# Optimization experiments

Measured on AMD Instinct MI355X. Metric: run time of the kernel, lower is better.

## Reference

```python
import jax, jax.numpy as jnp
import numpy as np

D_MODEL = 512
HEADS = 8
D_K = D_MODEL // HEADS
D_FF = 2048
SEQ = 2048
BATCH = 8


def setup_inputs() -> dict:
    key = jax.random.key(0)
    ks = jax.random.split(key, 16)
    xavier = lambda k, shape: jax.random.uniform(
        k, shape, jnp.float32,
        -jnp.sqrt(6.0 / (shape[-2] + shape[-1])), jnp.sqrt(6.0 / (shape[-2] + shape[-1])))
    inp = {
        'x': jax.random.normal(ks[0], (SEQ, BATCH, D_MODEL), jnp.float32),
        'Wq': xavier(ks[1], (D_MODEL, D_MODEL)), 'bq': jnp.zeros((D_MODEL,)),
        'Wv': xavier(ks[2], (D_MODEL, D_MODEL)), 'bv': jnp.zeros((D_MODEL,)),
        'Wr': xavier(ks[3], (D_MODEL, D_MODEL)), 'br': jnp.zeros((D_MODEL,)),
        'W_h': xavier(ks[4], (HEADS, D_K, D_K)),
        'Wo': xavier(ks[5], (D_MODEL, D_MODEL)),
        'bo': jax.random.normal(ks[6], (D_MODEL,)) * 0.01,
        'ln1_g': jnp.ones((D_MODEL,)), 'ln1_b': jnp.zeros((D_MODEL,)),
        'Wf1': xavier(ks[7], (D_MODEL, D_FF)), 'bf1': jnp.zeros((D_FF,)),
        'Wf2': xavier(ks[8], (D_FF, D_MODEL)), 'bf2': jnp.zeros((D_MODEL,)),
        'ln2_g': jnp.ones((D_MODEL,)), 'ln2_b': jnp.zeros((D_MODEL,)),
    }
    return inp


def _layernorm(x, g, b, eps=1e-5):
    mu = jnp.mean(x, axis=-1, keepdims=True)
    var = jnp.var(x, axis=-1, keepdims=True)
    return (x - mu) * jax.lax.rsqrt(var + eps) * g + b


def _forward(x, Wq, bq, Wv, bv, Wr, br, W_h, Wo, bo, ln1_g, ln1_b, Wf1, bf1, Wf2, bf2, ln2_g, ln2_b):
    S, B, D = x.shape
    # causal mask: triu bool ADDED to scores (torch quirk: bool->float gives +1.0)
    mask = jnp.triu(jnp.ones((S, S), jnp.float32), k=1)
    xt = jnp.transpose(x, (1, 0, 2))  # (B, S, D)
    Q = (xt @ Wq.T + bq).reshape(B, S, HEADS, D_K).transpose(0, 2, 1, 3)  # bhsd
    V = (xt @ Wv.T + bv).reshape(B, S, HEADS, D_K).transpose(0, 2, 1, 3)
    Rp = (xt @ Wr.T + br).reshape(B, S, HEADS, D_K).transpose(0, 2, 1, 3)
    # recurrence: h_t = tanh(einsum('hnk,bhn->bhn', W_h, h) + R_t)
    # note: einsum sums W_h over k per (h,n) -> elementwise scale by W_h.sum(-1)
    w_diag = jnp.sum(W_h, axis=-1)  # (H, D_K)

    def step(h, r_t):
        h_new = jnp.tanh(h * w_diag + r_t)
        return h_new, h_new

    h0 = jnp.zeros((B, HEADS, D_K), x.dtype)
    _, H = jax.lax.scan(step, h0, jnp.transpose(Rp, (2, 0, 1, 3)))  # (S,B,H,Dk)
    H = jnp.transpose(H, (1, 2, 0, 3))  # (B,H,S,Dk)
    scale = 1.0 / np.sqrt(D_K)
    scores = jnp.einsum('bhqd,bhkd->bhqk', Q, H) * scale + mask
    attn = jax.nn.softmax(scores, axis=-1)
    out = jnp.einsum('bhqk,bhkd->bhqd', attn, V)
    out = out.transpose(0, 2, 1, 3).reshape(B, S, D)
    attn_out = out @ Wo.T + bo
    attn_out = jnp.transpose(attn_out, (1, 0, 2))  # back to (S,B,D)
    x1 = _layernorm(x + attn_out, ln1_g, ln1_b)
    ff = jax.nn.relu(x1 @ Wf1) + 0.0
    ff = (jax.nn.relu(x1 @ Wf1 + bf1)) @ Wf2 + bf2
    return _layernorm(x1 + ff, ln2_g, ln2_b)


def reference(x, Wq, bq, Wv, bv, Wr, br, W_h, Wo, bo, ln1_g, ln1_b, Wf1, bf1, Wf2, bf2, ln2_g, ln2_b):
    return _forward(x, Wq, bq, Wv, bv, Wr, br, W_h, Wo, bo, ln1_g, ln1_b, Wf1, bf1, Wf2, bf2, ln2_g, ln2_b)
```

## Files before the change

### kernel.cpp

```cpp
#include <hip/hip_runtime.h>
#include <hip/hip_bf16.h>
#include <math.h>

#define SEQ    2048
#define BATCH  8
#define DMODEL 512
#define NHEADS 8
#define DK     64
#define DFF    2048
#define MROWS  16384

typedef __hip_bfloat16 bf16;
typedef unsigned int   u32;
typedef unsigned short u16;
typedef __attribute__((ext_vector_type(8))) short short8;
typedef __attribute__((ext_vector_type(4))) float f32x4;

#define LOG2E  1.4426950408889634f
#define LOG2E2 2.8853900817779268f
#define MC2    1.4426950408889634f

__device__ __forceinline__ float b2f(bf16 v) { return __bfloat162float(v); }
__device__ __forceinline__ bf16  f2b(float f) { return __float2bfloat16(f); }
__device__ __forceinline__ u16 f2u(float f) { bf16 h = __float2bfloat16(f); return *(u16*)&h; }
__device__ __forceinline__ u32 pack2(float a, float b) {
    return ((u32)f2u(b) << 16) | (u32)f2u(a);
}
__device__ __forceinline__ void unpack2(u32 u, float& a, float& b) {
    a = __uint_as_float(u << 16);
    b = __uint_as_float(u & 0xFFFF0000u);
}
__device__ __forceinline__ float ldE(const void* p, long off, int f32) {
    return f32 ? ((const float*)p)[off] : b2f(((const bf16*)p)[off]);
}
__device__ __forceinline__ void async16(bf16* lds, const bf16* g) {
    __builtin_amdgcn_global_load_lds(
        (const __attribute__((address_space(1))) void*)g,
        (__attribute__((address_space(3))) void*)lds, 16, 0, 0);
}

__global__ __launch_bounds__(256) void probe_kernel(const void* __restrict__ x,
                                                    int* __restrict__ flag)
{
    int tid = threadIdx.x;
    const u16* u = (const u16*)x;
    int cnt = 0;
    #pragma unroll
    for (int i = 0; i < 8; i++) {
        u16 e = u[tid * 8 + i];
        float v = __uint_as_float(((u32)e) << 16);
        float a = fabsf(v);
        if (a > 9.313226e-10f && a < 1.0737418e9f) cnt++;
    }
    __shared__ int sh[256];
    sh[tid] = cnt;
    __syncthreads();
    for (int s = 128; s > 0; s >>= 1) {
        if (tid < s) sh[tid] += sh[tid + s];
        __syncthreads();
    }
    if (tid == 0) *flag = (sh[0] < 1700) ? 1 : 0;
}

__global__ __launch_bounds__(256) void prep_all(
    const void* x, bf16* __restrict__ xb,
    const void* Wq, const void* Wv, const void* Wr, const void* Wo,
    const void* Wf1, const void* Wf2,
    const void* bq, const void* bv, const void* br, const void* bo,
    const void* bf1, const void* bf2,
    bf16* __restrict__ Wqvr, bf16* __restrict__ Wob,
    bf16* __restrict__ Wf1t, bf16* __restrict__ Wf2t,
    bf16* __restrict__ bqvr, bf16* __restrict__ bob,
    bf16* __restrict__ bf1b, bf16* __restrict__ bf2b,
    const int* __restrict__ flagp)
{
    const int f32 = *flagp;
    int bid = blockIdx.x;
    if (bid < 4096) {
        int gid = bid * 256 + threadIdx.x;
        int row_in = gid >> 6;
        int d8 = (gid & 63) * 8;
        int s = row_in >> 3, b = row_in & 7;
        long src = (long)row_in * 512 + d8;
        long dst = ((long)b * SEQ + s) * 512 + d8;
        if (f32) {
            const float* xf = (const float*)x;
            float4 a = *(const float4*)(xf + src);
            float4 c = *(const float4*)(xf + src + 4);
            u32 o[4] = { pack2(a.x,a.y), pack2(a.z,a.w), pack2(c.x,c.y), pack2(c.z,c.w) };
            *(uint4*)(xb + dst) = *(uint4*)o;
        } else {
            *(uint4*)(xb + dst) = *(const uint4*)((const bf16*)x + src);
        }
        return;
    }
    long g = (long)(bid - 4096) * 256 + threadIdx.x;
    if (g < 786432) {
        if (g < 262144) Wqvr[g] = f2b(ldE(Wq, g, f32) * LOG2E);
        else if (g < 524288) Wqvr[g] = f2b(ldE(Wv, g & 262143, f32));
        else Wqvr[g] = f2b(ldE(Wr, g & 262143, f32));
    } else if (g < 1048576) {
        long j = g - 786432;
        Wob[j] = f2b(ldE(Wo, j, f32));
    } else if (g < 2097152) {
        long j = g - 1048576;
        long n = j >> 9, k = j & 511;
        Wf1t[j] = f2b(ldE(Wf1, k * 2048 + n, f32));
    } else if (g < 3145728) {
        long j = g - 2097152;
        long n = j >> 11, k = j & 2047;
        Wf2t[j] = f2b(ldE(Wf2, k * 512 + n, f32));
    } else {
        long j = g - 3145728;
        if (j < 512)       bqvr[j]      = f2b(ldE(bq, j, f32) * LOG2E);
        else if (j < 1024) bqvr[j]      = f2b(ldE(bv, j - 512, f32));
        else if (j < 1536) bqvr[j]      = f2b(ldE(br, j - 1024, f32));
        else if (j < 2048) bob[j-1536]  = f2b(ldE(bo, j - 1536, f32));
        else if (j < 4096) bf1b[j-2048] = f2b(ldE(bf1, j - 2048, f32));
        else if (j < 4608) bf2b[j-4096] = f2b(ldE(bf2, j - 4096, f32));
    }
}

template<bool RELU>
__device__ __forceinline__ void gemm_body(
    const bf16* __restrict__ A, const bf16* __restrict__ W,
    const bf16* __restrict__ bias, bf16* __restrict__ C,
    int K, int lda, int ldc, int bx, int by, bf16* As, bf16* Bs)
{
    const int tid = threadIdx.x;
    const int w = tid >> 6, lane = tid & 63;
    const int li = lane & 15, quad = lane >> 4;
    const int m0 = bx * 128, n0 = by * 128;
    const int wm = (w >> 1) * 64, wn = (w & 1) * 64;
    const int srow = lane >> 2, scol = (lane & 3) * 8;

    f32x4 acc[4][4];
    const f32x4 z4 = {0.f, 0.f, 0.f, 0.f};
    #pragma unroll
    for (int i = 0; i < 4; i++)
        #pragma unroll
        for (int j = 0; j < 4; j++) acc[i][j] = z4;

    const bf16* ga = A + (long)(m0 + w * 32 + srow) * lda + scol;
    const bf16* gb = W + (long)(n0 + w * 32 + srow) * K + scol;
    bf16* lA0 = &As[(w * 32) * 32];
    bf16* lA1 = &As[(w * 32 + 16) * 32];
    bf16* lB0 = &Bs[(w * 32) * 32];
    bf16* lB1 = &Bs[(w * 32 + 16) * 32];

    for (int k0 = 0; k0 < K; k0 += 64) {
        __syncthreads();
        async16(lA0, ga);
        async16(lA1, ga + (long)16 * lda);
        async16(lA0 + 4096, ga + 32);
        async16(lA1 + 4096, ga + 32 + (long)16 * lda);
        async16(lB0, gb);
        async16(lB1, gb + (long)16 * K);
        async16(lB0 + 4096, gb + 32);
        async16(lB1 + 4096, gb + 32 + (long)16 * K);
        ga += 64; gb += 64;
        __syncthreads();
        #pragma unroll
        for (int ks = 0; ks < 2; ks++) {
            short8 af[4], bfr[4];
            #pragma unroll
            for (int t = 0; t < 4; t++)
                af[t] = *(const short8*)&As[ks * 4096 + (wm + t * 16 + li) * 32 + quad * 8];
            #pragma unroll
            for (int t = 0; t < 4; t++)
                bfr[t] = *(const short8*)&Bs[ks * 4096 + (wn + t * 16 + li) * 32 + quad * 8];
            #pragma unroll
            for (int i = 0; i < 4; i++)
                #pragma unroll
                for (int j = 0; j < 4; j++)
                    acc[i][j] = __builtin_amdgcn_mfma_f32_16x16x32_bf16(
                        af[i], bfr[j], acc[i][j], 0, 0, 0);
        }
    }

    #pragma unroll
    for (int i = 0; i < 4; i++) {
        #pragma unroll
        for (int j = 0; j < 4; j++) {
            int col = n0 + wn + j * 16 + li;
            float bb = b2f(bias[col]);
            #pragma unroll
            for (int r = 0; r < 4; r++) {
                int row = m0 + wm + i * 16 + quad * 4 + r;
                float v = acc[i][j][r] + bb;
                if (RELU) v = fmaxf(v, 0.f);
                C[(long)row * ldc + col] = f2b(v);
            }
        }
    }
}

template<bool RELU>
__global__ __launch_bounds__(256) void mfma_gemm(
    const bf16* __restrict__ A, const bf16* __restrict__ W,
    const bf16* __restrict__ bias, bf16* __restrict__ C,
    int K, int lda, int ldc)
{
    __shared__ bf16 As[8192];
    __shared__ bf16 Bs[8192];
    gemm_body<RELU>(A, W, bias, C, K, lda, ldc, blockIdx.x, blockIdx.y, As, Bs);
}

__global__ __launch_bounds__(256) void recur_par(bf16* __restrict__ QVR,
                                                 const void* __restrict__ Wh,
                                                 const int* __restrict__ flagp)
{
    const int f32 = *flagp;
    const int idx = blockIdx.x * 256 + threadIdx.x;
    const int k   = idx >> 12;
    const int rem = idx & 4095;
    const int b   = rem >> 9, o = rem & 511;

    float w = 0.0f;
    #pragma unroll
    for (int j = 0; j < DK; j++) w += ldE(Wh, (long)o * DK + j, f32);
    const float w2 = w * LOG2E2;

    const bf16* rb = QVR + (long)b * SEQ * 1536 + 1024 + o;
    bf16*       hb = QVR + (long)b * SEQ * 1536 + 512  + o;

    const int s1   = k * 128;
    const int s0   = (k == 0) ? 0 : s1 - 64;
    const int warm = s1 - s0;
    const int TOT  = 128 + warm;

    const int PF = 32;
    float buf[PF];
    #pragma unroll
    for (int i = 0; i < PF; i++)
        buf[i] = b2f(rb[(long)(s0 + i) * 1536]) * LOG2E2;

    float h = 0.0f;
    for (int t = 0; t < TOT; t += PF) {
        float nbuf[PF];
        if (t + PF < TOT) {
            #pragma unroll
            for (int i = 0; i < PF; i++)
                nbuf[i] = b2f(rb[(long)(s0 + t + PF + i) * 1536]) * LOG2E2;
        }
        const bool store = (t >= warm);
        #pragma unroll
        for (int i = 0; i < PF; i++) {
            float xx = fmaf(h, w2, buf[i]);
            float e  = __builtin_amdgcn_exp2f(xx);
            float d  = __builtin_amdgcn_rcpf(e + 1.0f);
            h = fmaf(-2.0f, d, 1.0f);
            if (store) hb[(long)(s0 + t + i) * 1536] = f2b(h * 0.125f);
        }
        #pragma unroll
        for (int i = 0; i < PF; i++) buf[i] = nbuf[i];
    }
}

__global__ __launch_bounds__(256) void vt_kernel(const bf16* __restrict__ QVR,
                                                 bf16* __restrict__ VTg)
{
    __shared__ bf16 Ls[64 * 72];
    int bh = blockIdx.y, b = bh >> 3, h = bh & 7;
    int s0 = blockIdx.x * 64;
    int t = threadIdx.x;
    #pragma unroll
    for (int i = 0; i < 2; i++) {
        int item = t + i * 256;
        int s = item >> 3, d8 = (item & 7) * 8;
        uint4 v = *(const uint4*)&QVR[((long)(b * SEQ + s0 + s)) * 1536 + 512 + h * 64 + d8];
        *(uint2*)&Ls[s * 72 + d8]     = make_uint2(v.x, v.y);
        *(uint2*)&Ls[s * 72 + d8 + 4] = make_uint2(v.z, v.w);
    }
    __syncthreads();
    #pragma unroll
    for (int i = 0; i < 2; i++) {
        int item = t + i * 256;
        int d = item >> 3, sg = item & 7;
        bf16 tmp[8];
        #pragma unroll
        for (int j = 0; j < 8; j++) tmp[j] = Ls[(sg * 8 + j) * 72 + d];
        int sgp = (sg & 4) | ((sg & 3) ^ ((d >> 3) & 3));
        *(uint4*)&VTg[((long)bh * 64 + d) * 2048 + s0 + sgp * 8] = *(uint4*)tmp;
    }
}

__global__ __launch_bounds__(512) void attn_mfma(const bf16* __restrict__ QVR,
                                                 const bf16* __restrict__ VTg,
                                                 bf16* __restrict__ O)
{
    __shared__ bf16 Kt[2][4096];
    __shared__ bf16 Vt[2][4096];
    __shared__ bf16 Pl[8 * 32 * 72];
    const int tid = threadIdx.x;
    const int w = tid >> 6, lane = tid & 63;
    const int li = lane & 15, quad = lane >> 4;
    const int bh = blockIdx.y;
    const int b = bh >> 3, hd = bh & 7;
    const int q0 = blockIdx.x * 256;
    const int qw = q0 + w * 32;
    const long rowb = (long)b * SEQ;
    const bf16* Qb = QVR + hd * DK;
    const bf16* Hb = QVR + 512 + hd * DK;
    bf16* Pw = &Pl[w * 32 * 72];
    const f32x4 z4 = {0.f, 0.f, 0.f, 0.f};

    short8 ones;
    #pragma unroll
    for (int i = 0; i < 8; i++) ones[i] = (short)0x3F80;

    short8 qa[2][2];
    #pragma unroll
    for (int mt = 0; mt < 2; mt++)
        #pragma unroll
        for (int ks = 0; ks < 2; ks++)
            qa[mt][ks] = *(const short8*)&Qb[(rowb + qw + mt * 16 + li) * 1536
                                             + ks * 32 + quad * 8];

    f32x4 oacc[2][4];
    f32x4 lacc[2];
    #pragma unroll
    for (int mt = 0; mt < 2; mt++) {
        #pragma unroll
        for (int dt = 0; dt < 4; dt++) oacc[mt][dt] = z4;
        lacc[mt] = z4;
    }

    const bf16* gk = Hb + (rowb + w * 16 + (lane >> 2)) * 1536 + (lane & 3) * 8;
    const bf16* gv = VTg + ((long)bh * 64 + (w - 4) * 16 + (lane >> 2)) * 2048
                     + (lane & 3) * 8;

    if (w < 4) {
        async16(&Kt[0][w * 512],        gk);
        async16(&Kt[0][2048 + w * 512], gk + 32);
    } else {
        async16(&Vt[0][(w - 4) * 512],        gv);
        async16(&Vt[0][2048 + (w - 4) * 512], gv + 32);
    }
    gk += (long)64 * 1536;
    gv += 64;
    __syncthreads();

    for (int t = 0; t < 32; t++) {
        const int cb = t & 1, nb = cb ^ 1;

        if (t < 31) {
            if (w < 4) {
                async16(&Kt[nb][w * 512],        gk);
                async16(&Kt[nb][2048 + w * 512], gk + 32);
            } else {
                async16(&Vt[nb][(w - 4) * 512],        gv);
                async16(&Vt[nb][2048 + (w - 4) * 512], gv + 32);
            }
            gk += (long)64 * 1536;
            gv += 64;
        }

        const int kt2 = t * 64;
        const bf16* Kp = Kt[cb];
        const bf16* Vp = Vt[cb];

        f32x4 sa[2][4];
        #pragma unroll
        for (int mt = 0; mt < 2; mt++)
            #pragma unroll
            for (int nt = 0; nt < 4; nt++) sa[mt][nt] = z4;
        #pragma unroll
        for (int ks = 0; ks < 2; ks++) {
            short8 kb[4];
            #pragma unroll
            for (int nt = 0; nt < 4; nt++)
                kb[nt] = *(const short8*)&Kp[ks * 2048 + (nt * 16 + li) * 32 + quad * 8];
            #pragma unroll
            for (int mt = 0; mt < 2; mt++)
                #pragma unroll
                for (int nt = 0; nt < 4; nt++)
                    sa[mt][nt] = __builtin_amdgcn_mfma_f32_16x16x32_bf16(
                        qa[mt][ks], kb[nt], sa[mt][nt], 0, 0, 0);
        }

        bool nomask  = (kt2 + 63 <= qw);
        bool allmask = (kt2 > qw + 31);
        if (nomask || allmask) {
            float MB = allmask ? MC2 : 0.0f;
            #pragma unroll
            for (int mt = 0; mt < 2; mt++)
                #pragma unroll
                for (int nt = 0; nt < 4; nt++) {
                    f32x4 s = sa[mt][nt];
                    #pragma unroll
                    for (int r = 0; r < 4; r++) {
                        float p = __builtin_amdgcn_exp2f(s[r] + MB);
                        Pw[(mt * 16 + quad * 4 + r) * 72 + nt * 16 + li] = f2b(p);
                    }
                }
        } else {
            #pragma unroll
            for (int mt = 0; mt < 2; mt++) {
                int qrow = qw + mt * 16 + quad * 4;
                #pragma unroll
                for (int nt = 0; nt < 4; nt++) {
                    int key = kt2 + nt * 16 + li;
                    f32x4 s = sa[mt][nt];
                    #pragma unroll
                    for (int r = 0; r < 4; r++) {
                        float arg = (key > qrow + r) ? s[r] + MC2 : s[r];
                        float p = __builtin_amdgcn_exp2f(arg);
                        Pw[(mt * 16 + quad * 4 + r) * 72 + nt * 16 + li] = f2b(p);
                    }
                }
            }
        }

        #pragma unroll
        for (int ks = 0; ks < 2; ks++) {
            short8 vbf[4], pa[2];
            #pragma unroll
            for (int dt = 0; dt < 4; dt++) {
                int d = dt * 16 + li;
                int sw = ((d >> 3) & 3) << 3;
                vbf[dt] = *(const short8*)&Vp[ks * 2048 + d * 32 + ((quad * 8) ^ sw)];
            }
            #pragma unroll
            for (int mt = 0; mt < 2; mt++)
                pa[mt] = *(const short8*)&Pw[(mt * 16 + li) * 72 + ks * 32 + quad * 8];
            #pragma unroll
            for (int mt = 0; mt < 2; mt++) {
                lacc[mt] = __builtin_amdgcn_mfma_f32_16x16x32_bf16(
                    pa[mt], ones, lacc[mt], 0, 0, 0);
                #pragma unroll
                for (int dt = 0; dt < 4; dt++)
                    oacc[mt][dt] = __builtin_amdgcn_mfma_f32_16x16x32_bf16(
                        pa[mt], vbf[dt], oacc[mt][dt], 0, 0, 0);
            }
        }

        __syncthreads();
    }

    #pragma unroll
    for (int mt = 0; mt < 2; mt++)
        #pragma unroll
        for (int r = 0; r < 4; r++) {
            float inv = 1.0f / lacc[mt][r];
            long row = rowb + qw + mt * 16 + quad * 4 + r;
            #pragma unroll
            for (int dt = 0; dt < 4; dt++)
                O[row * 512 + hd * 64 + dt * 16 + li] = f2b(oacc[mt][dt][r] * inv);
        }
}

__global__ __launch_bounds__(256) void ln1_kernel(const bf16* __restrict__ xb,
                                                  const bf16* __restrict__ ao,
                                                  const void* __restrict__ g,
                                                  const void* __restrict__ beta,
                                                  bf16* __restrict__ x1,
                                                  const int* __restrict__ flagp)
{
    const int f32 = *flagp;
    long base = (long)blockIdx.x * 512;
    int tid = threadIdx.x;
    int d2 = tid * 2;
    float x0, x1v, a0, a1;
    unpack2(*(const u32*)&xb[base + d2], x0, x1v);
    unpack2(*(const u32*)&ao[base + d2], a0, a1);
    float v0 = x0 + a0, v1 = x1v + a1;
    float s1 = v0 + v1;
    float s2 = v0 * v0 + v1 * v1;
    #pragma unroll
    for (int off = 32; off > 0; off >>= 1) {
        s1 += __shfl_down(s1, off);
        s2 += __shfl_down(s2, off);
    }
    __shared__ float w1[4], w2[4];
    int wid = tid >> 6, lane = tid & 63;
    if (lane == 0) { w1[wid] = s1; w2[wid] = s2; }
    __syncthreads();
    float t1 = w1[0] + w1[1] + w1[2] + w1[3];
    float t2 = w2[0] + w2[1] + w2[2] + w2[3];
    float mu = t1 * (1.0f / DMODEL);
    float var = t2 * (1.0f / DMODEL) - mu * mu;
    float rs = rsqrtf(var + 1e-5f);
    float r0 = (v0 - mu) * rs * ldE(g, d2, f32) + ldE(beta, d2, f32);
    float r1 = (v1 - mu) * rs * ldE(g, d2 + 1, f32) + ldE(beta, d2 + 1, f32);
    *(u32*)&x1[base + d2] = pack2(r0, r1);
}

__global__ __launch_bounds__(256) void ln2_kernel(const bf16* __restrict__ x1,
                                                  const bf16* __restrict__ ff2,
                                                  const void* __restrict__ g,
                                                  const void* __restrict__ beta,
                                                  void* __restrict__ outp,
                                                  const int* __restrict__ flagp)
{
    const int f32 = *flagp;
    int m = blockIdx.x;
    int b = m >> 11, s = m & 2047;
    long plain = (long)m * 512;
    long funny = ((long)s * BATCH + b) * 512;
    int tid = threadIdx.x;
    int d2 = tid * 2;
    float x0, x1v, a0, a1;
    unpack2(*(const u32*)&x1[plain + d2], x0, x1v);
    unpack2(*(const u32*)&ff2[plain + d2], a0, a1);
    float v0 = x0 + a0, v1 = x1v + a1;
    float s1 = v0 + v1;
    float s2 = v0 * v0 + v1 * v1;
    #pragma unroll
    for (int off = 32; off > 0; off >>= 1) {
        s1 += __shfl_down(s1, off);
        s2 += __shfl_down(s2, off);
    }
    __shared__ float w1[4], w2[4];
    int wid = tid >> 6, lane = tid & 63;
    if (lane == 0) { w1[wid] = s1; w2[wid] = s2; }
    __syncthreads();
    float t1 = w1[0] + w1[1] + w1[2] + w1[3];
    float t2 = w2[0] + w2[1] + w2[2] + w2[3];
    float mu = t1 * (1.0f / DMODEL);
    float var = t2 * (1.0f / DMODEL) - mu * mu;
    float rs = rsqrtf(var + 1e-5f);
    float r0 = (v0 - mu) * rs * ldE(g, d2, f32) + ldE(beta, d2, f32);
    float r1 = (v1 - mu) * rs * ldE(g, d2 + 1, f32) + ldE(beta, d2 + 1, f32);
    if (f32) {
        ((float*)outp)[funny + d2]     = r0;
        ((float*)outp)[funny + d2 + 1] = r1;
    } else {
        *(u32*)&((bf16*)outp)[funny + d2] = pack2(r0, r1);
    }
}

extern "C" void kernel_launch(void* const* d_in, const int* in_sizes, int n_in,
                              void* d_out, int out_size, void* d_ws, size_t ws_size,
                              hipStream_t stream)
{
    (void)in_sizes; (void)n_in; (void)out_size; (void)ws_size;
    const void* x = d_in[0];

    bf16* W    = (bf16*)d_ws;
    bf16* xb   = W;
    bf16* QVR  = W + (8u  << 20);
    bf16* Ob   = W + (32u << 20);
    bf16* VTg  = W + (40u << 20);
    bf16* AO   = W + (40u << 20);
    bf16* X1   = W + (8u  << 20);
    bf16* FFH  = W + (16u << 20);
    bf16* FF2  = W;
    int*  flag = (int*)((char*)d_ws + (size_t)96 * 1024 * 1024);
    bf16* Wt   = (bf16*)((char*)d_ws + (size_t)96 * 1024 * 1024 + 16);
    bf16* Wqvr = Wt;
    bf16* Wob  = Wt + 786432;
    bf16* Wf1t = Wt + 1048576;
    bf16* Wf2t = Wt + 2097152;
    bf16* bqvr = Wt + 3145728;
    bf16* bob  = Wt + 3147264;
    bf16* bf1b = Wt + 3147776;
    bf16* bf2b = Wt + 3149824;

    dim3 blk(256);
    probe_kernel<<<1, blk, 0, stream>>>(x, flag);
    prep_all<<<16402, blk, 0, stream>>>(
        x, xb,
        d_in[1], d_in[3], d_in[5], d_in[8], d_in[12], d_in[14],
        d_in[2], d_in[4], d_in[6], d_in[9], d_in[13], d_in[15],
        Wqvr, Wob, Wf1t, Wf2t, bqvr, bob, bf1b, bf2b, flag);

    mfma_gemm<false><<<dim3(128, 12), blk, 0, stream>>>(
        xb, Wqvr, bqvr, QVR, 512, 512, 1536);

    vt_kernel<<<dim3(32, 64), blk, 0, stream>>>(QVR, VTg);

    recur_par<<<256, blk, 0, stream>>>(QVR, d_in[7], flag);

    attn_mfma<<<dim3(8, 64), dim3(512), 0, stream>>>(QVR, VTg, Ob);

    mfma_gemm<false><<<dim3(128, 4), blk, 0, stream>>>(Ob, Wob, bob, AO, 512, 512, 512);

    ln1_kernel<<<MROWS, blk, 0, stream>>>(xb, AO, d_in[10], d_in[11], X1, flag);

    mfma_gemm<true><<<dim3(128, 16), blk, 0, stream>>>(X1, Wf1t, bf1b, FFH, 512, 512, 2048);

    mfma_gemm<false><<<dim3(128, 4), blk, 0, stream>>>(FFH, Wf2t, bf2b, FF2, 2048, 2048, 512);

    ln2_kernel<<<MROWS, blk, 0, stream>>>(X1, FF2, d_in[16], d_in[17], d_out, flag);
}
```

Baseline: 443.8 us.

## Load K and V fragments directly from global memory in attention kernel

```diff
diff --git a/kernel.cpp b/kernel.cpp
--- a/kernel.cpp
+++ b/kernel.cpp
@@ -280,8 +280,7 @@
         bf16 tmp[8];
         #pragma unroll
         for (int j = 0; j < 8; j++) tmp[j] = Ls[(sg * 8 + j) * 72 + d];
-        int sgp = (sg & 4) | ((sg & 3) ^ ((d >> 3) & 3));
-        *(uint4*)&VTg[((long)bh * 64 + d) * 2048 + s0 + sgp * 8] = *(uint4*)tmp;
+        *(uint4*)&VTg[((long)bh * 64 + d) * 2048 + s0 + sg * 8] = *(uint4*)tmp;
     }
 }
 
@@ -289,8 +288,6 @@
                                                  const bf16* __restrict__ VTg,
                                                  bf16* __restrict__ O)
 {
-    __shared__ bf16 Kt[2][4096];
-    __shared__ bf16 Vt[2][4096];
     __shared__ bf16 Pl[8 * 32 * 72];
     const int tid = threadIdx.x;
     const int w = tid >> 6, lane = tid & 63;
@@ -326,58 +323,32 @@
         lacc[mt] = z4;
     }
 
-    const bf16* gk = Hb + (rowb + w * 16 + (lane >> 2)) * 1536 + (lane & 3) * 8;
-    const bf16* gv = VTg + ((long)bh * 64 + (w - 4) * 16 + (lane >> 2)) * 2048
-                     + (lane & 3) * 8;
-
-    if (w < 4) {
-        async16(&Kt[0][w * 512],        gk);
-        async16(&Kt[0][2048 + w * 512], gk + 32);
-    } else {
-        async16(&Vt[0][(w - 4) * 512],        gv);
-        async16(&Vt[0][2048 + (w - 4) * 512], gv + 32);
-    }
-    gk += (long)64 * 1536;
-    gv += 64;
-    __syncthreads();
+    const bf16* gkb = Hb + (rowb + li) * 1536 + quad * 8;
+    const bf16* gvb = VTg + ((long)bh * 64 + li) * 2048 + quad * 8;
 
     for (int t = 0; t < 32; t++) {
-        const int cb = t & 1, nb = cb ^ 1;
-
-        if (t < 31) {
-            if (w < 4) {
-                async16(&Kt[nb][w * 512],        gk);
-                async16(&Kt[nb][2048 + w * 512], gk + 32);
-            } else {
-                async16(&Vt[nb][(w - 4) * 512],        gv);
-                async16(&Vt[nb][2048 + (w - 4) * 512], gv + 32);
-            }
-            gk += (long)64 * 1536;
-            gv += 64;
-        }
-
         const int kt2 = t * 64;
-        const bf16* Kp = Kt[cb];
-        const bf16* Vp = Vt[cb];
-
+
+        short8 kb[2][4];
+        #pragma unroll
+        for (int ks = 0; ks < 2; ks++)
+            #pragma unroll
+            for (int nt = 0; nt < 4; nt++)
+                kb[ks][nt] = *(const short8*)&gkb[(long)(kt2 + nt * 16) * 1536
+                                                  + ks * 32];
         f32x4 sa[2][4];
         #pragma unroll
         for (int mt = 0; mt < 2; mt++)
             #pragma unroll
             for (int nt = 0; nt < 4; nt++) sa[mt][nt] = z4;
         #pragma unroll
-        for (int ks = 0; ks < 2; ks++) {
-            short8 kb[4];
-            #pragma unroll
-            for (int nt = 0; nt < 4; nt++)
-                kb[nt] = *(const short8*)&Kp[ks * 2048 + (nt * 16 + li) * 32 + quad * 8];
+        for (int ks = 0; ks < 2; ks++)
             #pragma unroll
             for (int mt = 0; mt < 2; mt++)
                 #pragma unroll
                 for (int nt = 0; nt < 4; nt++)
                     sa[mt][nt] = __builtin_amdgcn_mfma_f32_16x16x32_bf16(
-                        qa[mt][ks], kb[nt], sa[mt][nt], 0, 0, 0);
-        }
+                        qa[mt][ks], kb[ks][nt], sa[mt][nt], 0, 0, 0);
 
         bool nomask  = (kt2 + 63 <= qw);
         bool allmask = (kt2 > qw + 31);
@@ -416,11 +387,9 @@
         for (int ks = 0; ks < 2; ks++) {
             short8 vbf[4], pa[2];
             #pragma unroll
-            for (int dt = 0; dt < 4; dt++) {
-                int d = dt * 16 + li;
-                int sw = ((d >> 3) & 3) << 3;
-                vbf[dt] = *(const short8*)&Vp[ks * 2048 + d * 32 + ((quad * 8) ^ sw)];
-            }
+            for (int dt = 0; dt < 4; dt++)
+                vbf[dt] = *(const short8*)&gvb[(long)(dt * 16) * 2048
+                                               + kt2 + ks * 32];
             #pragma unroll
             for (int mt = 0; mt < 2; mt++)
                 pa[mt] = *(const short8*)&Pw[(mt * 16 + li) * 72 + ks * 32 + quad * 8];
@@ -434,8 +403,6 @@
                         pa[mt], vbf[dt], oacc[mt][dt], 0, 0, 0);
             }
         }
-
-        __syncthreads();
     }
 
     #pragma unroll
```

New measurement: 570.3 us. 28.5% more time.
